# Kernel tuning notes

Measured on AMD Instinct MI355X. Metric: run time of the kernel, lower is better.

The kernel has to match this reference:

```python
import jax, jax.numpy as jnp
import numpy as np

B, H, V, T = 2048, 512, 64, 128

def setup_inputs() -> dict:
    key = jax.random.key(0)
    ks = jax.random.split(key, 7)
    s = 1.0 / np.sqrt(H)
    return {
        "z": jax.random.normal(ks[0], (B, H), dtype=jnp.float32),
        "w_ih": jax.random.uniform(ks[1], (4 * H, H), jnp.float32, -s, s),
        "w_hh": jax.random.uniform(ks[2], (4 * H, H), jnp.float32, -s, s),
        "b_ih": jax.random.uniform(ks[3], (4 * H,), jnp.float32, -s, s),
        "b_hh": jax.random.uniform(ks[4], (4 * H,), jnp.float32, -s, s),
        "fc_w": jax.random.uniform(ks[5], (V, H), jnp.float32, -s, s),
        "fc_b": jax.random.uniform(ks[6], (V,), jnp.float32, -s, s),
    }

def reference(z, w_ih, w_hh, b_ih, b_hh, fc_w, fc_b):
    batch = z.shape[0]
    # Input z is identical at every timestep -> precompute its gate contribution once.
    x_gates = z @ w_ih.T + b_ih + b_hh  # [B, 4H]

    def step(carry, _):
        h, c = carry
        gates = x_gates + h @ w_hh.T  # [B, 4H]
        i, f, g, o = jnp.split(gates, 4, axis=-1)  # PyTorch LSTMCell gate order
        i = jax.nn.sigmoid(i)
        f = jax.nn.sigmoid(f)
        g = jnp.tanh(g)
        o = jax.nn.sigmoid(o)
        c = f * c + i * g
        h = o * jnp.tanh(c)
        return (h, c), h

    h0 = jnp.zeros((batch, w_hh.shape[1]), dtype=z.dtype)
    c0 = jnp.zeros_like(h0)
    _, hs = jax.lax.scan(step, (h0, c0), None, length=T)  # [T, B, H]
    x = jnp.transpose(hs, (1, 0, 2))  # [B, T, H]
    return jax.nn.relu(x @ fc_w.T + fc_b)  # [B, T, V]
```

## Files before the change

kernel.cpp:

```cpp
#include <hip/hip_runtime.h>
#include <hip/hip_bf16.h>
#include <cstdint>

#define B_   2048
#define H_   512
#define T_   128
#define V_   64
#define FOURH 2048

typedef __bf16 bf16x8 __attribute__((ext_vector_type(8)));
typedef float  floatx4 __attribute__((ext_vector_type(4)));
typedef int    intx4   __attribute__((ext_vector_type(4)));
typedef int    intx2   __attribute__((ext_vector_type(2)));

__device__ __forceinline__ unsigned short f2bf(float f) {
    union { float f; uint32_t u; } v; v.f = f;
    uint32_t r = v.u + 0x7fff + ((v.u >> 16) & 1);
    return (unsigned short)(r >> 16);
}

__device__ __forceinline__ float rcp_(float x) {
    float r; asm("v_rcp_f32 %0, %1" : "=v"(r) : "v"(x)); return r;
}
__device__ __forceinline__ float sigmoidf_(float x) {
    return rcp_(1.0f + __expf(-x));
}
__device__ __forceinline__ float tanhf_(float x) {
    float e = __expf(fminf(-2.0f * x, 80.0f));
    return (1.0f - e) * rcp_(1.0f + e);
}

__device__ __forceinline__ void global_to_lds16(const unsigned short* g, unsigned short* l) {
    __builtin_amdgcn_global_load_lds(
        (const __attribute__((address_space(1))) unsigned int*)g,
        (__attribute__((address_space(3))) unsigned int*)l, 16, 0, 0);
}

__device__ __forceinline__ bf16x8 load16_sys(const unsigned short* p) {
    bf16x8 d;
    asm volatile("global_load_dwordx4 %0, %1, off sc0 sc1\n\t"
                 "s_waitcnt vmcnt(0)"
                 : "=v"(d) : "v"(p));
    return d;
}

__device__ __forceinline__ void flag_prefetch(const unsigned int* fp, intx4& f) {
    asm volatile("global_load_dwordx4 %0, %1, off sc0 sc1"
                 : "=v"(f) : "v"(fp) : "memory");
}
__device__ __forceinline__ bool flag_ok(const intx4& f, unsigned int tgt) {
    return (unsigned int)f[0] >= tgt && (unsigned int)f[1] >= tgt &&
           (unsigned int)f[2] >= tgt && (unsigned int)f[3] >= tgt;
}
__device__ __forceinline__ void wait4(const unsigned int* fp, unsigned int tgt) {
    for (;;) {
        intx4 f;
        asm volatile("global_load_dwordx4 %0, %1, off sc0 sc1\n\t"
                     "s_waitcnt vmcnt(0)" : "=v"(f) : "v"(fp) : "memory");
        if (flag_ok(f, tgt)) return;
        __builtin_amdgcn_s_sleep(1);
    }
}
__device__ __forceinline__ void flag_prefetch2(const unsigned int* fp, intx2& f) {
    asm volatile("global_load_dwordx2 %0, %1, off sc0 sc1"
                 : "=v"(f) : "v"(fp) : "memory");
}
__device__ __forceinline__ bool flag_ok2(const intx2& f, unsigned int tgt) {
    return (unsigned int)f[0] >= tgt && (unsigned int)f[1] >= tgt;
}
__device__ __forceinline__ void wait2(const unsigned int* fp, unsigned int tgt) {
    for (;;) {
        intx2 f;
        asm volatile("global_load_dwordx2 %0, %1, off sc0 sc1\n\t"
                     "s_waitcnt vmcnt(0)" : "=v"(f) : "v"(fp) : "memory");
        if (flag_ok2(f, tgt)) return;
        __builtin_amdgcn_s_sleep(1);
    }
}
__device__ __forceinline__ void flag_post(unsigned int* p, unsigned int v) {
    asm volatile("global_store_dword %0, %1, off sc0 sc1" :: "v"(p), "v"(v) : "memory");
}

__global__ void prep_kernel(const float* __restrict__ z,
                            const float* __restrict__ w_ih,
                            const float* __restrict__ w_hh,
                            const float* __restrict__ b_ih,
                            const float* __restrict__ b_hh,
                            const float* __restrict__ fc_w,
                            unsigned short* __restrict__ Bp_ih,
                            unsigned short* __restrict__ Bp_hh,
                            unsigned short* __restrict__ z_bf,
                            unsigned short* __restrict__ fcw_bf,
                            float* __restrict__ biasp,
                            unsigned int* __restrict__ cnt) {
    int i = blockIdx.x * blockDim.x + threadIdx.x;
    int col = i >> 9, k = i & 511;
    int jj = col >> 7, cc = col & 127;
    int gate = (cc >> 4) & 3;
    int hcl = ((cc >> 6) << 4) | (cc & 15);
    int p = gate * 512 + jj * 32 + hcl;
    Bp_hh[i] = f2bf(w_hh[p * 512 + k]);
    Bp_ih[i] = f2bf(w_ih[p * 512 + k]);
    z_bf[i]  = f2bf(z[i]);
    if (i < V_ * H_) fcw_bf[i] = f2bf(fc_w[i]);
    if (i < FOURH) {
        int j2 = i >> 7, c2 = i & 127;
        int g2 = (c2 >> 4) & 3;
        int h2 = ((c2 >> 6) << 4) | (c2 & 15);
        int p2 = g2 * 512 + j2 * 32 + h2;
        biasp[i] = b_ih[p2] + b_hh[p2];
    }
    if (i < 2048) cnt[i] = 0;
}

__device__ __forceinline__ void gemm_tile_r1(
        const unsigned short* __restrict__ Aglob,
        const unsigned short* __restrict__ Bglob,
        int arow0, int brow0,
        unsigned short* As, unsigned short* Bs,
        floatx4 acc[2][8], int w, int l) {
    const int lr = l >> 3;
    const int gl = (l & 7) ^ lr;
    const int ln = l & 15, lq = l >> 4, ls = l & 7;
    for (int kc = 0; kc < 8; ++kc) {
        const int kof = kc * 64 + gl * 8;
        #pragma unroll
        for (int q = 0; q < 4; ++q) {
            const int r0 = (w * 4 + q) * 8;
            global_to_lds16(Aglob + (size_t)(arow0 + r0 + lr) * 512 + kof, As + r0 * 64);
            global_to_lds16(Bglob + (size_t)(brow0 + r0 + lr) * 512 + kof, Bs + r0 * 64);
        }
        __syncthreads();
        #pragma unroll
        for (int kk = 0; kk < 2; ++kk) {
            bf16x8 a[2], b[8];
            #pragma unroll
            for (int mt = 0; mt < 2; ++mt) {
                const int m = 32 * w + 16 * mt + ln;
                const int g = kk * 4 + lq;
                a[mt] = *(const bf16x8*)(As + m * 64 + ((g ^ ls) * 8));
            }
            #pragma unroll
            for (int nt = 0; nt < 8; ++nt) {
                const int n = 16 * nt + ln;
                const int g = kk * 4 + lq;
                b[nt] = *(const bf16x8*)(Bs + n * 64 + ((g ^ ls) * 8));
            }
            #pragma unroll
            for (int mt = 0; mt < 2; ++mt)
                #pragma unroll
                for (int nt = 0; nt < 8; ++nt)
                    acc[mt][nt] = __builtin_amdgcn_mfma_f32_16x16x32_bf16(
                        a[mt], b[nt], acc[mt][nt], 0, 0, 0);
        }
        __syncthreads();
    }
}

__global__ void __launch_bounds__(256) xg_gemm_kernel(
        const unsigned short* __restrict__ z_bf,
        const unsigned short* __restrict__ Bp_ih,
        const float* __restrict__ biasp,
        float* __restrict__ xg) {
    __shared__ unsigned short As[128 * 64];
    __shared__ unsigned short Bs[128 * 64];
    const int bi = blockIdx.x, j = blockIdx.y;
    const int tid = threadIdx.x, w = tid >> 6, l = tid & 63;
    floatx4 acc[2][8];
    const floatx4 zf = {0.f, 0.f, 0.f, 0.f};
    for (int a1 = 0; a1 < 2; ++a1) for (int a2 = 0; a2 < 8; ++a2) acc[a1][a2] = zf;

    gemm_tile_r1(z_bf, Bp_ih, bi * 128, j * 128, As, Bs, acc, w, l);

    const int ln = l & 15, lq = l >> 4;
    #pragma unroll
    for (int mt = 0; mt < 2; ++mt)
        #pragma unroll
        for (int nt = 0; nt < 8; ++nt) {
            const int colp = j * 128 + nt * 16 + ln;
            const float bv = biasp[colp];
            #pragma unroll
            for (int r = 0; r < 4; ++r) {
                const int b = bi * 128 + 32 * w + 16 * mt + lq * 4 + r;
                xg[(size_t)b * FOURH + colp] = acc[mt][nt][r] + bv;
            }
        }
}

__device__ __forceinline__ void stage_issue2(const unsigned short* __restrict__ Aglob,
                                             int arow0, int kc, int w, int l,
                                             intx4& t0, intx4& t1) {
    const int lr = l >> 3;
    const int gl = (l & 7) ^ lr;
    const int kof = kc * 64 + gl * 8;
    const unsigned short* p0 = Aglob + (size_t)(arow0 + (w * 2 + 0) * 8 + lr) * 512 + kof;
    const unsigned short* p1 = Aglob + (size_t)(arow0 + (w * 2 + 1) * 8 + lr) * 512 + kof;
    asm volatile(
        "global_load_dwordx4 %0, %2, off sc0 sc1\n\t"
        "global_load_dwordx4 %1, %3, off sc0 sc1"
        : "=&v"(t0), "=&v"(t1)
        : "v"(p0), "v"(p1)
        : "memory");
}

__device__ __forceinline__ void commit4(unsigned short* buf, int w, int l,
                                        const intx4* u) {
    asm volatile("s_waitcnt vmcnt(0)" ::: "memory");
    const int lr = l >> 3, sl = (l & 7) * 8;
    #pragma unroll
    for (int kcL = 0; kcL < 2; ++kcL)
        #pragma unroll
        for (int q = 0; q < 2; ++q)
            *(intx4*)(buf + kcL * 4096 + ((w * 2 + q) * 8 + lr) * 64 + sl) = u[kcL * 2 + q];
}

__global__ void __launch_bounds__(256, 1) lstm_persistent(
        const unsigned short* __restrict__ Bp_hh,
        const unsigned short* __restrict__ fcw_bf,
        const float* __restrict__ xg,
        const float* __restrict__ fc_b,
        unsigned short* __restrict__ h0b,
        unsigned short* __restrict__ h1b,
        unsigned int* __restrict__ cnt,
        float* __restrict__ out) {
    __shared__ unsigned short AsB0[8192];
    __shared__ unsigned short AsB1[8192];

    const int bx = blockIdx.x;
    const int gi = bx & 31;
    const int j  = bx >> 5;
    const int tid = threadIdx.x;
    const int w = tid >> 6, l = tid & 63;
    const int ln = l & 15, lq = l >> 4;
    const bool jlt4 = (j < 4);
    const int j16 = j * 16;
    const int v = 16 * w + ln;
    const float fcb_v = fc_b[v];
    const int arow0 = gi * 64;
    const int colbase = j * 256 + (w >> 1) * 128 + (w & 1) * 64;
    unsigned int* flagp = cnt + gi * 64;
    const floatx4 zf = {0.f, 0.f, 0.f, 0.f};

    bf16x8 bq[16][4];
    {
        const unsigned short* bbase =
            Bp_hh + ((size_t)(colbase + ln)) * 512 + lq * 8;
        #pragma unroll
        for (int s = 0; s < 16; ++s)
            #pragma unroll
            for (int nt = 0; nt < 4; ++nt)
                bq[s][nt] = *(const bf16x8*)(bbase + (size_t)nt * 16 * 512 + s * 32);
    }

    floatx4 xga[4][4];
    #pragma unroll
    for (int mt = 0; mt < 4; ++mt)
        #pragma unroll
        for (int nt = 0; nt < 4; ++nt)
            #pragma unroll
            for (int r = 0; r < 4; ++r) {
                const int b = arow0 + 16 * mt + lq * 4 + r;
                xga[mt][nt][r] = xg[(size_t)b * FOURH + colbase + 16 * nt + ln];
            }

    unsigned short* hlds = AsB0;

    float cst[4][4];
    #pragma unroll
    for (int mt = 0; mt < 4; ++mt)
        #pragma unroll
        for (int r = 0; r < 4; ++r) {
            float iv = sigmoidf_(xga[mt][0][r]);
            float gv = tanhf_  (xga[mt][2][r]);
            float ov = sigmoidf_(xga[mt][3][r]);
            float cv = iv * gv;
            cst[mt][r] = cv;
            hlds[(16 * mt + lq * 4 + r) * 64 + (16 * w + ln)] = f2bf(ov * tanhf_(cv));
        }
    __syncthreads();
    for (int c = tid; c < 512; c += 256) {
        const int row = c >> 3, seg = c & 7;
        intx4 d = *(const intx4*)(hlds + row * 64 + seg * 8);
        const unsigned short* p = h0b + (size_t)(arow0 + row) * 512 + j * 64 + seg * 8;
        asm volatile("global_store_dwordx4 %0, %1, off sc0 sc1" :: "v"(p), "v"(d) : "memory");
    }
    asm volatile("s_waitcnt vmcnt(0)" ::: "memory");
    __syncthreads();
    if (tid == 0) flag_post(flagp + j, 1u);
    intx2 fpre2;
    flag_prefetch2(flagp, fpre2);

    unsigned short* hb[2] = {h0b, h1b};
    #pragma unroll 1
    for (int t = 1; t < T_; ++t) {
        const unsigned int tg = (unsigned int)t;

        asm volatile("s_waitcnt vmcnt(0)" ::: "memory");
        __builtin_amdgcn_sched_barrier(0);
        if (!flag_ok2(fpre2, tg)) wait2(flagp, tg);

        const unsigned short* hprev = hb[(t - 1) & 1];
        unsigned short* hnext = hb[t & 1];

        floatx4 acc[4][4];
        #pragma unroll
        for (int a1 = 0; a1 < 4; ++a1)
            #pragma unroll
            for (int a2 = 0; a2 < 4; ++a2) acc[a1][a2] = zf;
        floatx4 pacc = zf;

        intx4 u[4];
        stage_issue2(hprev, arow0, 0, w, l, u[0], u[1]);
        stage_issue2(hprev, arow0, 1, w, l, u[2], u[3]);
        flag_prefetch2(flagp + 2, fpre2);
        commit4(AsB0, w, l, u);
        __syncthreads();

        #pragma unroll
        for (int g = 0; g < 4; ++g) {
            if (g < 3) {
                __builtin_amdgcn_sched_barrier(0);
                if (!flag_ok2(fpre2, tg)) wait2(flagp + 2 * (g + 1), tg);
                stage_issue2(hprev, arow0, 2 * g + 2, w, l, u[0], u[1]);
                stage_issue2(hprev, arow0, 2 * g + 3, w, l, u[2], u[3]);
                if (g < 2) flag_prefetch2(flagp + 2 * (g + 2), fpre2);
            }
            const unsigned short* buf = (g & 1) ? AsB1 : AsB0;
            #pragma unroll
            for (int ss = 0; ss < 4; ++ss) {
                const int s = g * 4 + ss;
                const int ga = (ss & 1) * 4 + lq;
                const unsigned short* Ac = buf + (ss >> 1) * 4096;
                bf16x8 af[4];
                #pragma unroll
                for (int mt = 0; mt < 4; ++mt) {
                    const int m = 16 * mt + ln;
                    af[mt] = *(const bf16x8*)(Ac + m * 64 + ((ga ^ (ln & 7)) * 8));
                }
                #pragma unroll
                for (int mt = 0; mt < 4; ++mt)
                    #pragma unroll
                    for (int nt = 0; nt < 4; ++nt)
                        acc[mt][nt] = __builtin_amdgcn_mfma_f32_16x16x32_bf16(
                            af[mt], bq[s][nt], acc[mt][nt], 0, 0, 0);
                if (jlt4) {
                    bf16x8 ap = *(const bf16x8*)(Ac + (j16 + ln) * 64 + ((ga ^ (ln & 7)) * 8));
                    bf16x8 bp = *(const bf16x8*)(fcw_bf + (size_t)v * 512 + s * 32 + lq * 8);
                    pacc = __builtin_amdgcn_mfma_f32_16x16x32_bf16(ap, bp, pacc, 0, 0, 0);
                }
            }
            if (g < 3) {
                commit4((g & 1) ? AsB0 : AsB1, w, l, u);
                __syncthreads();
            }
        }

        #pragma unroll
        for (int mt = 0; mt < 4; ++mt)
            #pragma unroll
            for (int r = 0; r < 4; ++r) {
                float iv = sigmoidf_(acc[mt][0][r] + xga[mt][0][r]);
                float fv = sigmoidf_(acc[mt][1][r] + xga[mt][1][r]);
                float gv = tanhf_  (acc[mt][2][r] + xga[mt][2][r]);
                float ov = sigmoidf_(acc[mt][3][r] + xga[mt][3][r]);
                float cn = fv * cst[mt][r] + iv * gv;
                cst[mt][r] = cn;
                hlds[(16 * mt + lq * 4 + r) * 64 + (16 * w + ln)] = f2bf(ov * tanhf_(cn));
            }
        __syncthreads();
        for (int c = tid; c < 512; c += 256) {
            const int row = c >> 3, seg = c & 7;
            intx4 d = *(const intx4*)(hlds + row * 64 + seg * 8);
            const unsigned short* p = hnext + (size_t)(arow0 + row) * 512 + j * 64 + seg * 8;
            asm volatile("global_store_dwordx4 %0, %1, off sc0 sc1" :: "v"(p), "v"(d) : "memory");
        }
        asm volatile("s_waitcnt vmcnt(0)" ::: "memory");
        __syncthreads();
        if (tid == 0) flag_post(flagp + j, tg + 1u);
        flag_prefetch2(flagp, fpre2);

        if (jlt4) {
            #pragma unroll
            for (int r = 0; r < 4; ++r) {
                const int b = arow0 + j16 + lq * 4 + r;
                out[(size_t)b * (T_ * V_) + (t - 1) * V_ + v] = fmaxf(pacc[r] + fcb_v, 0.0f);
            }
        }
    }

    if (jlt4) {
        wait4(flagp,     T_);
        wait4(flagp + 4, T_);
        const unsigned short* hlast = hb[(T_ - 1) & 1];
        floatx4 pa = zf;
        const int ar = arow0 + j16 + ln;
        #pragma unroll
        for (int kc = 0; kc < 16; ++kc) {
            const int k = kc * 32 + lq * 8;
            bf16x8 a = load16_sys(hlast + (size_t)ar * 512 + k);
            bf16x8 b = *(const bf16x8*)(fcw_bf + (size_t)v * 512 + k);
            pa = __builtin_amdgcn_mfma_f32_16x16x32_bf16(a, b, pa, 0, 0, 0);
        }
        #pragma unroll
        for (int r = 0; r < 4; ++r) {
            const int b = arow0 + j16 + lq * 4 + r;
            out[(size_t)b * (T_ * V_) + (T_ - 1) * V_ + v] = fmaxf(pa[r] + fcb_v, 0.0f);
        }
    }
}

extern "C" void kernel_launch(void* const* d_in, const int* in_sizes, int n_in,
                              void* d_out, int out_size, void* d_ws, size_t ws_size,
                              hipStream_t stream) {
    const float* z    = (const float*)d_in[0];
    const float* w_ih = (const float*)d_in[1];
    const float* w_hh = (const float*)d_in[2];
    const float* b_ih = (const float*)d_in[3];
    const float* b_hh = (const float*)d_in[4];
    const float* fc_w = (const float*)d_in[5];
    const float* fc_b = (const float*)d_in[6];
    float* out = (float*)d_out;

    char* ws = (char*)d_ws;
    size_t o = 0;
    auto take = [&](size_t bytes) { char* p = ws + o; o += (bytes + 255) & ~(size_t)255; return p; };
    unsigned short* Bp_hh  = (unsigned short*)take((size_t)FOURH * H_ * 2);
    unsigned short* Bp_ih  = (unsigned short*)take((size_t)FOURH * H_ * 2);
    unsigned short* z_bf   = (unsigned short*)take((size_t)B_ * H_ * 2);
    unsigned short* fcw_bf = (unsigned short*)take((size_t)V_ * H_ * 2);
    float*          biasp  = (float*)take((size_t)FOURH * 4);
    unsigned short* hbuf0  = (unsigned short*)take((size_t)B_ * H_ * 2);
    unsigned short* hbuf1  = (unsigned short*)take((size_t)B_ * H_ * 2);
    unsigned int*   cnt    = (unsigned int*)take(32 * 256);
    float*          xg     = (float*)take((size_t)B_ * FOURH * 4);

    prep_kernel<<<(B_ * H_) / 256, 256, 0, stream>>>(z, w_ih, w_hh, b_ih, b_hh, fc_w,
                                                     Bp_ih, Bp_hh, z_bf, fcw_bf, biasp, cnt);
    xg_gemm_kernel<<<dim3(16, 16), 256, 0, stream>>>(z_bf, Bp_ih, biasp, xg);
    lstm_persistent<<<256, 256, 0, stream>>>(Bp_hh, fcw_bf, xg, fc_b,
                                             hbuf0, hbuf1, cnt, out);
}
```

Before: 1.563 ms.

## Issue all h_prev loads upfront after waiting on all eight flags

Measured after the change: 1.525 ms. 2.4% less time.

```diff
diff --git a/kernel.cpp b/kernel.cpp
--- a/kernel.cpp
+++ b/kernel.cpp
@@ -11,7 +11,6 @@
 typedef __bf16 bf16x8 __attribute__((ext_vector_type(8)));
 typedef float  floatx4 __attribute__((ext_vector_type(4)));
 typedef int    intx4   __attribute__((ext_vector_type(4)));
-typedef int    intx2   __attribute__((ext_vector_type(2)));
 
 __device__ __forceinline__ unsigned short f2bf(float f) {
     union { float f; uint32_t u; } v; v.f = f;
@@ -58,22 +57,6 @@
         asm volatile("global_load_dwordx4 %0, %1, off sc0 sc1\n\t"
                      "s_waitcnt vmcnt(0)" : "=v"(f) : "v"(fp) : "memory");
         if (flag_ok(f, tgt)) return;
-        __builtin_amdgcn_s_sleep(1);
-    }
-}
-__device__ __forceinline__ void flag_prefetch2(const unsigned int* fp, intx2& f) {
-    asm volatile("global_load_dwordx2 %0, %1, off sc0 sc1"
-                 : "=v"(f) : "v"(fp) : "memory");
-}
-__device__ __forceinline__ bool flag_ok2(const intx2& f, unsigned int tgt) {
-    return (unsigned int)f[0] >= tgt && (unsigned int)f[1] >= tgt;
-}
-__device__ __forceinline__ void wait2(const unsigned int* fp, unsigned int tgt) {
-    for (;;) {
-        intx2 f;
-        asm volatile("global_load_dwordx2 %0, %1, off sc0 sc1\n\t"
-                     "s_waitcnt vmcnt(0)" : "=v"(f) : "v"(fp) : "memory");
-        if (flag_ok2(f, tgt)) return;
         __builtin_amdgcn_s_sleep(1);
     }
 }
@@ -203,9 +186,13 @@
         : "memory");
 }
 
-__device__ __forceinline__ void commit4(unsigned short* buf, int w, int l,
-                                        const intx4* u) {
-    asm volatile("s_waitcnt vmcnt(0)" ::: "memory");
+template<int N>
+__device__ __forceinline__ void commit4c(unsigned short* buf, int w, int l,
+                                         const intx4* u) {
+    if constexpr (N == 12) asm volatile("s_waitcnt vmcnt(12)" ::: "memory");
+    else if constexpr (N == 8)  asm volatile("s_waitcnt vmcnt(8)"  ::: "memory");
+    else if constexpr (N == 4)  asm volatile("s_waitcnt vmcnt(4)"  ::: "memory");
+    else                        asm volatile("s_waitcnt vmcnt(0)"  ::: "memory");
     const int lr = l >> 3, sl = (l & 7) * 8;
     #pragma unroll
     for (int kcL = 0; kcL < 2; ++kcL)
@@ -223,8 +210,8 @@
         unsigned short* __restrict__ h1b,
         unsigned int* __restrict__ cnt,
         float* __restrict__ out) {
-    __shared__ unsigned short AsB0[8192];
-    __shared__ unsigned short AsB1[8192];
+    __shared__ unsigned short AsB0[4096 * 2];
+    __shared__ unsigned short AsB1[4096 * 2];
 
     const int bx = blockIdx.x;
     const int gi = bx & 31;
@@ -287,8 +274,9 @@
     asm volatile("s_waitcnt vmcnt(0)" ::: "memory");
     __syncthreads();
     if (tid == 0) flag_post(flagp + j, 1u);
-    intx2 fpre2;
-    flag_prefetch2(flagp, fpre2);
+    intx4 fpreA, fpreB;
+    flag_prefetch(flagp,     fpreA);
+    flag_prefetch(flagp + 4, fpreB);
 
     unsigned short* hb[2] = {h0b, h1b};
     #pragma unroll 1
@@ -297,7 +285,10 @@
 
         asm volatile("s_waitcnt vmcnt(0)" ::: "memory");
         __builtin_amdgcn_sched_barrier(0);
-        if (!flag_ok2(fpre2, tg)) wait2(flagp, tg);
+        if (!(flag_ok(fpreA, tg) && flag_ok(fpreB, tg))) {
+            wait4(flagp, tg);
+            wait4(flagp + 4, tg);
+        }
 
         const unsigned short* hprev = hb[(t - 1) & 1];
         unsigned short* hnext = hb[t & 1];
@@ -309,22 +300,17 @@
             for (int a2 = 0; a2 < 4; ++a2) acc[a1][a2] = zf;
         floatx4 pacc = zf;
 
-        intx4 u[4];
-        stage_issue2(hprev, arow0, 0, w, l, u[0], u[1]);
-        stage_issue2(hprev, arow0, 1, w, l, u[2], u[3]);
-        flag_prefetch2(flagp + 2, fpre2);
-        commit4(AsB0, w, l, u);
+        intx4 u[16];
+        #pragma unroll
+        for (int g = 0; g < 4; ++g) {
+            stage_issue2(hprev, arow0, 2 * g,     w, l, u[4 * g + 0], u[4 * g + 1]);
+            stage_issue2(hprev, arow0, 2 * g + 1, w, l, u[4 * g + 2], u[4 * g + 3]);
+        }
+        commit4c<12>(AsB0, w, l, &u[0]);
         __syncthreads();
 
         #pragma unroll
         for (int g = 0; g < 4; ++g) {
-            if (g < 3) {
-                __builtin_amdgcn_sched_barrier(0);
-                if (!flag_ok2(fpre2, tg)) wait2(flagp + 2 * (g + 1), tg);
-                stage_issue2(hprev, arow0, 2 * g + 2, w, l, u[0], u[1]);
-                stage_issue2(hprev, arow0, 2 * g + 3, w, l, u[2], u[3]);
-                if (g < 2) flag_prefetch2(flagp + 2 * (g + 2), fpre2);
-            }
             const unsigned short* buf = (g & 1) ? AsB1 : AsB0;
             #pragma unroll
             for (int ss = 0; ss < 4; ++ss) {
@@ -349,10 +335,9 @@
                     pacc = __builtin_amdgcn_mfma_f32_16x16x32_bf16(ap, bp, pacc, 0, 0, 0);
                 }
             }
-            if (g < 3) {
-                commit4((g & 1) ? AsB0 : AsB1, w, l, u);
-                __syncthreads();
-            }
+            if (g == 0) { commit4c<8>(AsB1, w, l, &u[4]);  __syncthreads(); }
+            else if (g == 1) { commit4c<4>(AsB0, w, l, &u[8]);  __syncthreads(); }
+            else if (g == 2) { commit4c<0>(AsB1, w, l, &u[12]); __syncthreads(); }
         }
 
         #pragma unroll
@@ -377,7 +362,8 @@
         asm volatile("s_waitcnt vmcnt(0)" ::: "memory");
         __syncthreads();
         if (tid == 0) flag_post(flagp + j, tg + 1u);
-        flag_prefetch2(flagp, fpre2);
+        flag_prefetch(flagp,     fpreA);
+        flag_prefetch(flagp + 4, fpreB);
 
         if (jlt4) {
             #pragma unroll
```
